# Optimization experiments

Hardware: AMD Instinct MI355X
Metric: run time of the kernel (lower is better)

Reference implementation:

```python
import jax, jax.numpy as jnp
import numpy as np

N_HEAD = 16
LOCAL_CTX = 256
W_SCALE = 0.02  # keep logits in a sane range, like trained-net init


def setup_inputs() -> dict:
    key = jax.random.key(0)
    k1, k2, k3 = jax.random.split(key, 3)
    B, T, C = 4, 2048, 1024
    x = jax.random.normal(k1, (B, T, C), dtype=jnp.float32)
    W_attn = jax.random.normal(k2, (C, 3 * C), dtype=jnp.float32) * W_SCALE
    b_attn = jnp.zeros((3 * C,), dtype=jnp.float32)
    W_proj = jax.random.normal(k3, (C, C), dtype=jnp.float32) * W_SCALE
    b_proj = jnp.zeros((C,), dtype=jnp.float32)
    return {"x": x, "W_attn": W_attn, "b_attn": b_attn,
            "W_proj": W_proj, "b_proj": b_proj}


def _local_causal_mask(T, ctx):
    # token i attends to j with j <= i and i - j < ctx  (band of width ctx)
    i = jnp.arange(T)[:, None]
    j = jnp.arange(T)[None, :]
    ctx = min(T, ctx)
    return (j <= i) & ((i - j) < ctx)  # [T, T] bool


def reference(x, W_attn, b_attn, W_proj, b_proj):
    B, T, C = x.shape
    H = N_HEAD
    D = C // H
    qkv = x @ W_attn + b_attn                       # [B, T, 3C]
    q, k, v = jnp.split(qkv, 3, axis=-1)
    q = q.reshape(B, T, H, D).transpose(0, 2, 1, 3)  # [B, H, T, D]
    k = k.reshape(B, T, H, D).transpose(0, 2, 1, 3)
    v = v.reshape(B, T, H, D).transpose(0, 2, 1, 3)
    scale = 1.0 / jnp.sqrt(jnp.asarray(D, dtype=x.dtype))
    w = jnp.einsum('bhtd,bhsd->bhts', q, k) * scale  # [B, H, T, T]
    mask = _local_causal_mask(T, LOCAL_CTX)          # [T, T]
    w = jnp.where(mask[None, None], w, -jnp.inf)
    p = jax.nn.softmax(w, axis=-1)
    a = jnp.einsum('bhts,bhsd->bhtd', p, v)          # [B, H, T, D]
    y = a.transpose(0, 2, 1, 3).reshape(B, T, C)
    return y @ W_proj + b_proj
```

## Files before the change

### kernel.cpp

```cpp
#include <hip/hip_runtime.h>
#include <stdint.h>

#define B_SZ 4
#define T_SEQ 2048
#define C_DIM 1024
#define NH 16
#define DH 64
#define CTX 256

#define AS_G const __attribute__((address_space(1))) void*
#define AS_L __attribute__((address_space(3))) void*

typedef __attribute__((ext_vector_type(8))) short bf16x8;
typedef __attribute__((ext_vector_type(8))) unsigned short u16x8;
typedef __attribute__((ext_vector_type(4))) unsigned short u16x4;
typedef __attribute__((ext_vector_type(2))) unsigned int u32x2;
typedef __attribute__((ext_vector_type(4))) float f32x4;

__device__ __forceinline__ float bf2f(unsigned short u) {
  unsigned int x = ((unsigned int)u) << 16;
  return __builtin_bit_cast(float, x);
}
__device__ __forceinline__ unsigned short f2bf(float f) {
  unsigned int u = __builtin_bit_cast(unsigned int, f);
  u = (u + 0x7FFFu + ((u >> 16) & 1u)) >> 16;
  return (unsigned short)u;
}
__device__ __forceinline__ unsigned int cvtpk(float lo, float hi) {
  unsigned int r;
  asm("v_cvt_pk_bf16_f32 %0, %1, %2" : "=v"(r) : "v"(lo), "v"(hi));
  return r;
}


__global__ void cvt_f32_bf16(const float* __restrict__ in,
                             unsigned short* __restrict__ out, int n8) {
  int i = blockIdx.x * blockDim.x + threadIdx.x;
  int stride = gridDim.x * blockDim.x;
  for (; i < n8; i += stride) {
    float4 a = ((const float4*)in)[2 * (size_t)i];
    float4 b = ((const float4*)in)[2 * (size_t)i + 1];
    u16x8 r;
    r[0] = f2bf(a.x); r[1] = f2bf(a.y); r[2] = f2bf(a.z); r[3] = f2bf(a.w);
    r[4] = f2bf(b.x); r[5] = f2bf(b.y); r[6] = f2bf(b.z); r[7] = f2bf(b.w);
    *(u16x8*)(out + 8 * (size_t)i) = r;
  }
}

__global__ void transpose_cvt(const float* __restrict__ W,
                              unsigned short* __restrict__ Wt, int R, int CC) {
  __shared__ float tile[32][33];
  int ct = blockIdx.x, rt = blockIdx.y;
  int tx = threadIdx.x & 31, ty = threadIdx.x >> 5;
#pragma unroll
  for (int i = 0; i < 4; ++i) {
    int r = ty + i * 8;
    tile[r][tx] = W[(size_t)(rt * 32 + r) * CC + ct * 32 + tx];
  }
  __syncthreads();
#pragma unroll
  for (int i = 0; i < 4; ++i) {
    int r = ty + i * 8;
    Wt[(size_t)(ct * 32 + r) * R + rt * 32 + tx] = f2bf(tile[tx][r]);
  }
}

#define BM 128
#define BN 128
#define BK 64

__global__ __launch_bounds__(256) void gemm_bt(
    const unsigned short* __restrict__ A, const unsigned short* __restrict__ Bt,
    const float* __restrict__ bias, int N, int K, int mode,
    float* __restrict__ outF, unsigned short* __restrict__ Qb,
    unsigned short* __restrict__ Kb, unsigned short* __restrict__ VTb) {
  __shared__ unsigned short As[BM * BK];
  __shared__ unsigned short Bs[BN * BK];
  const int tid = threadIdx.x;
  const int lane = tid & 63;
  const int w = tid >> 6;
  const int wm = w >> 1, wn = w & 1;
  const int m0 = blockIdx.y * BM, n0 = blockIdx.x * BN;

  const int srow = lane >> 3;
  const int sgch = (lane & 7) ^ srow;

  f32x4 acc[4][4];
#pragma unroll
  for (int mi = 0; mi < 4; ++mi)
#pragma unroll
    for (int ni = 0; ni < 4; ++ni) acc[mi][ni] = (f32x4){0.f, 0.f, 0.f, 0.f};

  for (int k0 = 0; k0 < K; k0 += BK) {
#pragma unroll
    for (int i = 0; i < 4; ++i) {
      int r8 = w * 4 + i;
      int row = r8 * 8 + srow;
      __builtin_amdgcn_global_load_lds(
          (AS_G)&A[(size_t)(m0 + row) * K + k0 + sgch * 8],
          (AS_L)((__attribute__((address_space(3))) unsigned short*)As + r8 * 512),
          16, 0, 0);
      __builtin_amdgcn_global_load_lds(
          (AS_G)&Bt[(size_t)(n0 + row) * K + k0 + sgch * 8],
          (AS_L)((__attribute__((address_space(3))) unsigned short*)Bs + r8 * 512),
          16, 0, 0);
    }
    __syncthreads();
#pragma unroll
    for (int ks = 0; ks < 2; ++ks) {
      bf16x8 av[4], bv[4];
      const int colc = (ks << 2) + (lane >> 4);
#pragma unroll
      for (int mi = 0; mi < 4; ++mi) {
        int row = wm * 64 + mi * 16 + (lane & 15);
        av[mi] = *(const bf16x8*)&As[row * BK + ((colc ^ (row & 7)) << 3)];
      }
#pragma unroll
      for (int ni = 0; ni < 4; ++ni) {
        int row = wn * 64 + ni * 16 + (lane & 15);
        bv[ni] = *(const bf16x8*)&Bs[row * BK + ((colc ^ (row & 7)) << 3)];
      }
#pragma unroll
      for (int mi = 0; mi < 4; ++mi)
#pragma unroll
        for (int ni = 0; ni < 4; ++ni)
          acc[mi][ni] = __builtin_amdgcn_mfma_f32_16x16x32_bf16(
              av[mi], bv[ni], acc[mi][ni], 0, 0, 0);
    }
    __syncthreads();
  }

#pragma unroll
  for (int mi = 0; mi < 4; ++mi) {
#pragma unroll
    for (int ni = 0; ni < 4; ++ni) {
      int gn = n0 + wn * 64 + ni * 16 + (lane & 15);
      float bb = bias[gn];
      int gmb = m0 + wm * 64 + mi * 16 + ((lane >> 4) << 2);
      if (mode == 0) {
#pragma unroll
        for (int j = 0; j < 4; ++j)
          outF[(size_t)(gmb + j) * N + gn] = acc[mi][ni][j] + bb;
      } else {
        int sec = gn >> 10, cc = gn & 1023;
        int h = cc >> 6, d = cc & 63;
        int b = gmb >> 11, t = gmb & 2047;
        if (sec == 2) {
          u16x4 pk;
#pragma unroll
          for (int j = 0; j < 4; ++j) pk[j] = f2bf(acc[mi][ni][j] + bb);
          *(u16x4*)&VTb[((size_t)(b * NH + h) * DH + d) * T_SEQ + t] = pk;
        } else {
          size_t dst = (((size_t)(b * NH + h) * T_SEQ) + t) * DH + d;
          float sc = (sec == 0) ? 0.125f : 1.0f;
          unsigned short* P = (sec == 0) ? Qb : Kb;
#pragma unroll
          for (int j = 0; j < 4; ++j)
            P[dst + (size_t)j * DH] = f2bf((acc[mi][ni][j] + bb) * sc);
        }
      }
    }
  }
}

__global__ __launch_bounds__(512, 4) void attn_mfma(
    const unsigned short* __restrict__ Qb,
    const unsigned short* __restrict__ Kb,
    const unsigned short* __restrict__ VT,
    unsigned short* __restrict__ Ab) {
  __shared__ unsigned short Ks[64 * 64];
  __shared__ unsigned short Vs[64 * 64];
  __shared__ unsigned short Pb[8][16][40];
  const int tid = threadIdx.x;
  const int w = tid >> 6, lane = tid & 63;
  const int lo = lane & 15, hi = lane >> 4;
  const int bh = blockIdx.x >> 4;
  const int t0 = (blockIdx.x & 15) * 128;
  const int b = bh >> 4, h = bh & 15;
  const size_t base = (size_t)bh * (T_SEQ * DH);
  const int t0w = t0 + 16 * w;
  const int tq = t0w + lo;
  const int sw = lo & 7;

  const int srow = tid >> 3;
  const int sgch = (tid & 7) ^ (srow & 7);

  const unsigned short* qp = Qb + base + (size_t)tq * DH + hi * 8;
  bf16x8 qa0 = *(const bf16x8*)qp;
  bf16x8 qa1 = *(const bf16x8*)(qp + 32);

  f32x4 O[4];
#pragma unroll
  for (int f = 0; f < 4; ++f) O[f] = (f32x4){0.f, 0.f, 0.f, 0.f};
  float lsum = 0.f;

  int kb_start = t0 - 256;
  if (kb_start < 0) kb_start = 0;
  const int kb_end = t0 + 128;

  for (int kb = kb_start; kb < kb_end; kb += 64) {
    __builtin_amdgcn_global_load_lds(
        (AS_G)&Kb[base + (size_t)(kb + srow) * DH + sgch * 8],
        (AS_L)((__attribute__((address_space(3))) unsigned short*)Ks + w * 512),
        16, 0, 0);
    __builtin_amdgcn_global_load_lds(
        (AS_G)&VT[base + (size_t)srow * T_SEQ + kb + sgch * 8],
        (AS_L)((__attribute__((address_space(3))) unsigned short*)Vs + w * 512),
        16, 0, 0);
    __syncthreads();

#pragma unroll
    for (int sb = 0; sb < 2; ++sb) {
      const int kbs = kb + 32 * sb;
      if (kbs > t0w + 15 || kbs + 31 < t0w - 255) continue;

      const int r0 = 32 * sb + lo, r1 = r0 + 16;
      bf16x8 kc0a = *(const bf16x8*)&Ks[r0 * 64 + ((hi ^ sw) << 3)];
      bf16x8 kc0b = *(const bf16x8*)&Ks[r0 * 64 + (((hi + 4) ^ sw) << 3)];
      bf16x8 kc1a = *(const bf16x8*)&Ks[r1 * 64 + ((hi ^ sw) << 3)];
      bf16x8 kc1b = *(const bf16x8*)&Ks[r1 * 64 + (((hi + 4) ^ sw) << 3)];

      f32x4 s0 = __builtin_amdgcn_mfma_f32_16x16x32_bf16(
          kc0a, qa0, (f32x4){0.f, 0.f, 0.f, 0.f}, 0, 0, 0);
      s0 = __builtin_amdgcn_mfma_f32_16x16x32_bf16(kc0b, qa1, s0, 0, 0, 0);
      f32x4 s1 = __builtin_amdgcn_mfma_f32_16x16x32_bf16(
          kc1a, qa0, (f32x4){0.f, 0.f, 0.f, 0.f}, 0, 0, 0);
      s1 = __builtin_amdgcn_mfma_f32_16x16x32_bf16(kc1b, qa1, s1, 0, 0, 0);

      float p[8];
      const bool full = (kbs >= t0w - 240) && (kbs + 31 <= t0w);
      if (full) {
#pragma unroll
        for (int j = 0; j < 4; ++j) {
          p[j] = __expf(s0[j]);
          p[4 + j] = __expf(s1[j]);
        }
      } else {
#pragma unroll
        for (int j = 0; j < 4; ++j) {
          int key = kbs + 4 * hi + j;
          p[j] = ((unsigned)(tq - key) < 256u) ? __expf(s0[j]) : 0.f;
          p[4 + j] = ((unsigned)(tq - key - 16) < 256u) ? __expf(s1[j]) : 0.f;
        }
      }
      lsum += ((p[0] + p[1]) + (p[2] + p[3])) + ((p[4] + p[5]) + (p[6] + p[7]));

      u32x2 w0, w1;
      w0[0] = cvtpk(p[0], p[1]); w0[1] = cvtpk(p[2], p[3]);
      w1[0] = cvtpk(p[4], p[5]); w1[1] = cvtpk(p[6], p[7]);
      *(u32x2*)&Pb[w][lo][4 * hi] = w0;
      *(u32x2*)&Pb[w][lo][16 + 4 * hi] = w1;

      bf16x8 pa = *(const bf16x8*)&Pb[w][lo][hi * 8];
#pragma unroll
      for (int dt = 0; dt < 4; ++dt) {
        int vd = dt * 16 + lo;
        bf16x8 vf =
            *(const bf16x8*)&Vs[vd * 64 + (((sb * 4 + hi) ^ sw) << 3)];
        O[dt] = __builtin_amdgcn_mfma_f32_16x16x32_bf16(vf, pa, O[dt], 0, 0, 0);
      }
    }
    __syncthreads();
  }

  lsum += __shfl_xor(lsum, 16);
  lsum += __shfl_xor(lsum, 32);
  float inv = 1.f / lsum;
  size_t ob = ((size_t)(b * T_SEQ + tq)) * C_DIM + h * DH + 4 * hi;
#pragma unroll
  for (int dt = 0; dt < 4; ++dt) {
    u16x4 o;
#pragma unroll
    for (int j = 0; j < 4; ++j) o[j] = f2bf(O[dt][j] * inv);
    *(u16x4*)&Ab[ob + dt * 16] = o;
  }
}


extern "C" void kernel_launch(void* const* d_in, const int* in_sizes, int n_in,
                              void* d_out, int out_size, void* d_ws, size_t ws_size,
                              hipStream_t stream) {
  const float* x = (const float*)d_in[0];
  const float* Wa = (const float*)d_in[1];
  const float* ba = (const float*)d_in[2];
  const float* Wp = (const float*)d_in[3];
  const float* bp = (const float*)d_in[4];
  float* out = (float*)d_out;
  char* ws = (char*)d_ws;

  unsigned short* xb  = (unsigned short*)(ws);
  unsigned short* WaT = (unsigned short*)(ws + (16u << 20));
  unsigned short* WpT = (unsigned short*)(ws + (22u << 20));
  unsigned short* Qb  = (unsigned short*)(ws + (24u << 20));
  unsigned short* Kb  = (unsigned short*)(ws + (40u << 20));
  unsigned short* VT  = (unsigned short*)(ws + (56u << 20));
  unsigned short* Ab  = xb;

  cvt_f32_bf16<<<2048, 256, 0, stream>>>(x, xb, (B_SZ * T_SEQ * C_DIM) / 8);
  transpose_cvt<<<dim3(96, 32), 256, 0, stream>>>(Wa, WaT, C_DIM, 3 * C_DIM);
  transpose_cvt<<<dim3(32, 32), 256, 0, stream>>>(Wp, WpT, C_DIM, C_DIM);
  gemm_bt<<<dim3(3 * C_DIM / BN, B_SZ * T_SEQ / BM), 256, 0, stream>>>(
      xb, WaT, ba, 3 * C_DIM, C_DIM, 1, nullptr, Qb, Kb, VT);
  attn_mfma<<<B_SZ * NH * T_SEQ / 128, 512, 0, stream>>>(Qb, Kb, VT, Ab);
  gemm_bt<<<dim3(C_DIM / BN, B_SZ * T_SEQ / BM), 256, 0, stream>>>(
      Ab, WpT, bp, C_DIM, C_DIM, 0, out, nullptr, nullptr, nullptr);
}
```

Measured before the change: 137.7 us.

## Double-buffer attention K/V tiles, raise MFMA priority, use packed bf16 converts

The attention kernel now double-buffers its K and V LDS tiles. It issues the async global-to-LDS load for the next 64-key chunk before computing on the current one, so load latency overlaps the MFMA work and one barrier per chunk is dropped. s_setprio is raised around the MFMA sequences to favour matrix issue across waves. Float-to-bf16 conversion in the convert, QKV-epilogue and attention-output paths switches from the manual rounding routine to the packed v_cvt_pk_bf16_f32 instruction. In exchange, attention LDS use doubles, which may reduce occupancy.

```diff
diff --git a/kernel.cpp b/kernel.cpp
--- a/kernel.cpp
+++ b/kernel.cpp
@@ -15,6 +15,7 @@
 typedef __attribute__((ext_vector_type(8))) unsigned short u16x8;
 typedef __attribute__((ext_vector_type(4))) unsigned short u16x4;
 typedef __attribute__((ext_vector_type(2))) unsigned int u32x2;
+typedef __attribute__((ext_vector_type(4))) unsigned int u32x4;
 typedef __attribute__((ext_vector_type(4))) float f32x4;
 
 __device__ __forceinline__ float bf2f(unsigned short u) {
@@ -40,10 +41,10 @@
   for (; i < n8; i += stride) {
     float4 a = ((const float4*)in)[2 * (size_t)i];
     float4 b = ((const float4*)in)[2 * (size_t)i + 1];
-    u16x8 r;
-    r[0] = f2bf(a.x); r[1] = f2bf(a.y); r[2] = f2bf(a.z); r[3] = f2bf(a.w);
-    r[4] = f2bf(b.x); r[5] = f2bf(b.y); r[6] = f2bf(b.z); r[7] = f2bf(b.w);
-    *(u16x8*)(out + 8 * (size_t)i) = r;
+    u32x4 r;
+    r[0] = cvtpk(a.x, a.y); r[1] = cvtpk(a.z, a.w);
+    r[2] = cvtpk(b.x, b.y); r[3] = cvtpk(b.z, b.w);
+    *(u32x4*)(out + 8 * (size_t)i) = r;
   }
 }
 
@@ -146,17 +147,23 @@
         int h = cc >> 6, d = cc & 63;
         int b = gmb >> 11, t = gmb & 2047;
         if (sec == 2) {
-          u16x4 pk;
-#pragma unroll
-          for (int j = 0; j < 4; ++j) pk[j] = f2bf(acc[mi][ni][j] + bb);
-          *(u16x4*)&VTb[((size_t)(b * NH + h) * DH + d) * T_SEQ + t] = pk;
+          u32x2 pk;
+          pk[0] = cvtpk(acc[mi][ni][0] + bb, acc[mi][ni][1] + bb);
+          pk[1] = cvtpk(acc[mi][ni][2] + bb, acc[mi][ni][3] + bb);
+          *(u32x2*)&VTb[((size_t)(b * NH + h) * DH + d) * T_SEQ + t] = pk;
         } else {
           size_t dst = (((size_t)(b * NH + h) * T_SEQ) + t) * DH + d;
           float sc = (sec == 0) ? 0.125f : 1.0f;
+          float bbs = bb * sc;
           unsigned short* P = (sec == 0) ? Qb : Kb;
-#pragma unroll
-          for (int j = 0; j < 4; ++j)
-            P[dst + (size_t)j * DH] = f2bf((acc[mi][ni][j] + bb) * sc);
+          unsigned int a = cvtpk(fmaf(acc[mi][ni][0], sc, bbs),
+                                 fmaf(acc[mi][ni][1], sc, bbs));
+          unsigned int c = cvtpk(fmaf(acc[mi][ni][2], sc, bbs),
+                                 fmaf(acc[mi][ni][3], sc, bbs));
+          P[dst] = (unsigned short)a;
+          P[dst + DH] = (unsigned short)(a >> 16);
+          P[dst + 2 * DH] = (unsigned short)c;
+          P[dst + 3 * DH] = (unsigned short)(c >> 16);
         }
       }
     }
@@ -168,8 +175,8 @@
     const unsigned short* __restrict__ Kb,
     const unsigned short* __restrict__ VT,
     unsigned short* __restrict__ Ab) {
-  __shared__ unsigned short Ks[64 * 64];
-  __shared__ unsigned short Vs[64 * 64];
+  __shared__ unsigned short Ks[2][64 * 64];
+  __shared__ unsigned short Vs[2][64 * 64];
   __shared__ unsigned short Pb[8][16][40];
   const int tid = threadIdx.x;
   const int w = tid >> 6, lane = tid & 63;
@@ -197,17 +204,28 @@
   int kb_start = t0 - 256;
   if (kb_start < 0) kb_start = 0;
   const int kb_end = t0 + 128;
-
-  for (int kb = kb_start; kb < kb_end; kb += 64) {
+  const int nch = (kb_end - kb_start) >> 6;
+
+  auto STAGE = [&](int kb, int bi) {
     __builtin_amdgcn_global_load_lds(
         (AS_G)&Kb[base + (size_t)(kb + srow) * DH + sgch * 8],
-        (AS_L)((__attribute__((address_space(3))) unsigned short*)Ks + w * 512),
+        (AS_L)((__attribute__((address_space(3))) unsigned short*)Ks[bi] +
+               w * 512),
         16, 0, 0);
     __builtin_amdgcn_global_load_lds(
         (AS_G)&VT[base + (size_t)srow * T_SEQ + kb + sgch * 8],
-        (AS_L)((__attribute__((address_space(3))) unsigned short*)Vs + w * 512),
+        (AS_L)((__attribute__((address_space(3))) unsigned short*)Vs[bi] +
+               w * 512),
         16, 0, 0);
-    __syncthreads();
+  };
+
+  STAGE(kb_start, 0);
+  __syncthreads();
+
+  for (int ci = 0; ci < nch; ++ci) {
+    const int kb = kb_start + (ci << 6);
+    const int cb = ci & 1;
+    if (ci + 1 < nch) STAGE(kb + 64, cb ^ 1);
 
 #pragma unroll
     for (int sb = 0; sb < 2; ++sb) {
@@ -215,17 +233,19 @@
       if (kbs > t0w + 15 || kbs + 31 < t0w - 255) continue;
 
       const int r0 = 32 * sb + lo, r1 = r0 + 16;
-      bf16x8 kc0a = *(const bf16x8*)&Ks[r0 * 64 + ((hi ^ sw) << 3)];
-      bf16x8 kc0b = *(const bf16x8*)&Ks[r0 * 64 + (((hi + 4) ^ sw) << 3)];
-      bf16x8 kc1a = *(const bf16x8*)&Ks[r1 * 64 + ((hi ^ sw) << 3)];
-      bf16x8 kc1b = *(const bf16x8*)&Ks[r1 * 64 + (((hi + 4) ^ sw) << 3)];
-
+      bf16x8 kc0a = *(const bf16x8*)&Ks[cb][r0 * 64 + ((hi ^ sw) << 3)];
+      bf16x8 kc0b = *(const bf16x8*)&Ks[cb][r0 * 64 + (((hi + 4) ^ sw) << 3)];
+      bf16x8 kc1a = *(const bf16x8*)&Ks[cb][r1 * 64 + ((hi ^ sw) << 3)];
+      bf16x8 kc1b = *(const bf16x8*)&Ks[cb][r1 * 64 + (((hi + 4) ^ sw) << 3)];
+
+      __builtin_amdgcn_s_setprio(1);
       f32x4 s0 = __builtin_amdgcn_mfma_f32_16x16x32_bf16(
           kc0a, qa0, (f32x4){0.f, 0.f, 0.f, 0.f}, 0, 0, 0);
       s0 = __builtin_amdgcn_mfma_f32_16x16x32_bf16(kc0b, qa1, s0, 0, 0, 0);
       f32x4 s1 = __builtin_amdgcn_mfma_f32_16x16x32_bf16(
           kc1a, qa0, (f32x4){0.f, 0.f, 0.f, 0.f}, 0, 0, 0);
       s1 = __builtin_amdgcn_mfma_f32_16x16x32_bf16(kc1b, qa1, s1, 0, 0, 0);
+      __builtin_amdgcn_s_setprio(0);
 
       float p[8];
       const bool full = (kbs >= t0w - 240) && (kbs + 31 <= t0w);
@@ -252,13 +272,15 @@
       *(u32x2*)&Pb[w][lo][16 + 4 * hi] = w1;
 
       bf16x8 pa = *(const bf16x8*)&Pb[w][lo][hi * 8];
+      __builtin_amdgcn_s_setprio(1);
 #pragma unroll
       for (int dt = 0; dt < 4; ++dt) {
         int vd = dt * 16 + lo;
         bf16x8 vf =
-            *(const bf16x8*)&Vs[vd * 64 + (((sb * 4 + hi) ^ sw) << 3)];
+            *(const bf16x8*)&Vs[cb][vd * 64 + (((sb * 4 + hi) ^ sw) << 3)];
         O[dt] = __builtin_amdgcn_mfma_f32_16x16x32_bf16(vf, pa, O[dt], 0, 0, 0);
       }
+      __builtin_amdgcn_s_setprio(0);
     }
     __syncthreads();
   }
@@ -269,10 +291,10 @@
   size_t ob = ((size_t)(b * T_SEQ + tq)) * C_DIM + h * DH + 4 * hi;
 #pragma unroll
   for (int dt = 0; dt < 4; ++dt) {
-    u16x4 o;
-#pragma unroll
-    for (int j = 0; j < 4; ++j) o[j] = f2bf(O[dt][j] * inv);
-    *(u16x4*)&Ab[ob + dt * 16] = o;
+    u32x2 o;
+    o[0] = cvtpk(O[dt][0] * inv, O[dt][1] * inv);
+    o[1] = cvtpk(O[dt][2] * inv, O[dt][3] * inv);
+    *(u32x2*)&Ab[ob + dt * 16] = o;
   }
 }
 
```

Measured after the change: 137.5 us. About the same (-0.2%).
